# Performance work log

Hardware: AMD Instinct MI355X
Metric: run time of the kernel (lower is better)

## Reference

```python
import jax, jax.numpy as jnp
import numpy as np

D = 2048
H = 16
HD = D // H  # 128


def setup_inputs() -> dict:
    key = jax.random.key(0)
    k1, k2, k3 = jax.random.split(key, 3)
    x = jax.random.normal(k1, (2, 2048, D), dtype=jnp.float32)
    # nn.Linear(d, 3d, bias=False): weight [3d, d]; y = x @ W.T
    w_qkv = jax.random.normal(k2, (3 * D, D), dtype=jnp.float32) * (1.0 / np.sqrt(D))
    w_o = jax.random.normal(k3, (D, D), dtype=jnp.float32) * (1.0 / np.sqrt(D))
    return {"x": x, "w_qkv": w_qkv, "w_o": w_o}


def reference(x, w_qkv, w_o):
    B, T, _ = x.shape
    qkv = jnp.einsum('btd,ed->bte', x, w_qkv)  # [B,T,3D]
    q, k, v = jnp.split(qkv, 3, axis=-1)
    # [B,T,D] -> [B,H,T,hd]
    q = q.reshape(B, T, H, HD).transpose(0, 2, 1, 3)
    k = k.reshape(B, T, H, HD).transpose(0, 2, 1, 3)
    v = v.reshape(B, T, H, HD).transpose(0, 2, 1, 3)
    att = jnp.einsum('bhtd,bhsd->bhts', q, k) / np.sqrt(HD).astype(np.float32)
    att = jax.nn.softmax(att, axis=-1)
    y = jnp.einsum('bhts,bhsd->bhtd', att, v)
    y = y.transpose(0, 2, 1, 3).reshape(B, T, D)
    return jnp.einsum('btd,ed->bte', y, w_o)
```

## Files before the change

### kernel.cpp

```cpp
#include <hip/hip_runtime.h>
#include <hip/hip_bf16.h>
#include <math.h>

typedef __bf16 bf16_t;
typedef __attribute__((ext_vector_type(8))) __bf16 bx8;
typedef __attribute__((ext_vector_type(4))) __bf16 bx4;
typedef __attribute__((ext_vector_type(4))) short sx4;
typedef __attribute__((ext_vector_type(4))) float fx4;

#define DEV __device__ __forceinline__

DEV void async_copy16(void* lds, const void* g) {
    __builtin_amdgcn_global_load_lds(
        (const __attribute__((address_space(1))) unsigned int*)g,
        (__attribute__((address_space(3))) unsigned int*)lds, 16, 0, 0);
}

DEV fx4 mfma16(bx4 a, bx4 b, fx4 c) {
#if __has_builtin(__builtin_amdgcn_mfma_f32_16x16x16bf16_1k)
    return __builtin_amdgcn_mfma_f32_16x16x16bf16_1k(
        __builtin_bit_cast(sx4, a), __builtin_bit_cast(sx4, b), c, 0, 0, 0);
#elif __has_builtin(__builtin_amdgcn_mfma_f32_16x16x16_bf16)
    return __builtin_amdgcn_mfma_f32_16x16x16_bf16(a, b, c, 0, 0, 0);
#else
    asm("v_mfma_f32_16x16x16_bf16 %0, %1, %2, %0" : "+v"(c) : "v"(a), "v"(b));
    return c;
#endif
}

__global__ void __launch_bounds__(256) cvt_all(const float* __restrict__ x,
                                               const float* __restrict__ wq,
                                               const float* __restrict__ wo,
                                               bf16_t* __restrict__ xb,
                                               bf16_t* __restrict__ wqb,
                                               bf16_t* __restrict__ wob) {
    int i = (blockIdx.x * 256 + threadIdx.x) * 4;
    const float* in;
    bf16_t* out;
    int k;
    if (i < 8388608) { in = x; out = xb; k = i; }
    else if (i < 8388608 + 12582912) { in = wq; out = wqb; k = i - 8388608; }
    else { in = wo; out = wob; k = i - (8388608 + 12582912); }
    float4 v = *(const float4*)(in + k);
    bx4 o = { (__bf16)v.x, (__bf16)v.y, (__bf16)v.z, (__bf16)v.w };
    *(bx4*)(out + k) = o;
}

template <bool BF16_OUT>
__global__ void __launch_bounds__(256, 2) gemm_bt(const bf16_t* __restrict__ A,
                                                  const bf16_t* __restrict__ B,
                                                  void* __restrict__ C,
                                                  bf16_t* __restrict__ VP,
                                                  int M, int N, int K, float scale0) {
    __shared__ bf16_t As[2 * 4096];
    __shared__ bf16_t Bs[2 * 4096];
    const int tid = threadIdx.x;
    const int w = tid >> 6, lane = tid & 63;
    const int ln = lane & 15, quad = lane >> 4;
    const int m0 = blockIdx.y * 128, n0 = blockIdx.x * 128;
    const int wm = (w >> 1) * 64, wn = (w & 1) * 64;
    const float scale = (n0 < 2048) ? scale0 : 1.0f;

    fx4 acc[4][4];
#pragma unroll
    for (int i = 0; i < 4; ++i)
#pragma unroll
        for (int j = 0; j < 4; ++j) acc[i][j] = (fx4){0.f, 0.f, 0.f, 0.f};

    for (int k0 = 0; k0 < K; k0 += 64) {
#pragma unroll
        for (int call = 0; call < 4; ++call) {
            int c = w * 256 + call * 64 + lane;
            int p = c >> 9, row = (c >> 2) & 127, piece = c & 3;
            async_copy16(As + (size_t)(w * 256 + call * 64) * 8,
                         A + (size_t)(m0 + row) * K + k0 + p * 32 + piece * 8);
            async_copy16(Bs + (size_t)(w * 256 + call * 64) * 8,
                         B + (size_t)(n0 + row) * K + k0 + p * 32 + piece * 8);
        }
        __syncthreads();

#pragma unroll
        for (int kk = 0; kk < 2; ++kk) {
            bx8 af[4], bf[4];
#pragma unroll
            for (int i = 0; i < 4; ++i)
                af[i] = *(const bx8*)(As + (size_t)kk * 4096 + (wm + i * 16 + ln) * 32 + quad * 8);
#pragma unroll
            for (int j = 0; j < 4; ++j)
                bf[j] = *(const bx8*)(Bs + (size_t)kk * 4096 + (wn + j * 16 + ln) * 32 + quad * 8);
#pragma unroll
            for (int i = 0; i < 4; ++i)
#pragma unroll
                for (int j = 0; j < 4; ++j)
                    acc[i][j] = __builtin_amdgcn_mfma_f32_16x16x32_bf16(af[i], bf[j], acc[i][j], 0, 0, 0);
        }
        __syncthreads();
    }

    if (VP != nullptr && n0 >= 4096) {
        const int h = (n0 - 4096) >> 7;
        const int bidx = m0 >> 11;
        bf16_t* vpb = VP + (size_t)(bidx * 16 + h) * 262144;
        const int key_base = (m0 & 2047) + wm;
#pragma unroll
        for (int i = 0; i < 4; ++i) {
            int key = key_base + i * 16 + quad * 4;
#pragma unroll
            for (int j = 0; j < 4; ++j) {
                int hd = wn + j * 16 + ln;
                bx4 v = { (__bf16)acc[i][j][0], (__bf16)acc[i][j][1],
                          (__bf16)acc[i][j][2], (__bf16)acc[i][j][3] };
                *(bx4*)(vpb + (size_t)(key >> 2) * 512 + hd * 4) = v;
            }
        }
    } else {
#pragma unroll
        for (int i = 0; i < 4; ++i) {
            int mrow = m0 + wm + i * 16 + quad * 4;
#pragma unroll
            for (int j = 0; j < 4; ++j) {
                int ncol = n0 + wn + j * 16 + ln;
#pragma unroll
                for (int r = 0; r < 4; ++r) {
                    if (BF16_OUT)
                        ((bf16_t*)C)[(size_t)(mrow + r) * N + ncol] = (__bf16)(acc[i][j][r] * scale);
                    else
                        ((float*)C)[(size_t)(mrow + r) * N + ncol] = acc[i][j][r];
                }
            }
        }
    }
}

__global__ void __launch_bounds__(256, 2) attn(const bf16_t* __restrict__ qkv,
                                               const bf16_t* __restrict__ vp,
                                               bf16_t* __restrict__ y) {
    __shared__ bf16_t Ks[128 * 128];
    __shared__ bf16_t Vs[16384];
    const int tid = threadIdx.x;
    const int w = tid >> 6, lane = tid & 63;
    const int ln = lane & 15, quad = lane >> 4;
    const int lin = blockIdx.x;
    const int slot = lin >> 3;
    const int bh = (lin & 7) + ((slot >> 4) << 3);
    const int qt = slot & 15;
    const int b = bh >> 4, h = bh & 15;

    const bf16_t* Qb = qkv + (size_t)(b * 2048 + qt * 128) * 6144 + h * 128;
    const bf16_t* Kb = qkv + (size_t)(b * 2048) * 6144 + 2048 + h * 128;
    const bf16_t* VPb = vp + (size_t)bh * 262144;

    bx8 qf[2][4];
#pragma unroll
    for (int i = 0; i < 2; ++i)
#pragma unroll
        for (int kk = 0; kk < 4; ++kk)
            qf[i][kk] = *(const bx8*)(Qb + (size_t)(w * 32 + i * 16 + ln) * 6144 + kk * 32 + quad * 8);

    const __bf16 one = (__bf16)1.0f;
    const bx4 ones4 = { one, one, one, one };

    fx4 o[2][8];
#pragma unroll
    for (int i = 0; i < 2; ++i)
#pragma unroll
        for (int j = 0; j < 8; ++j) o[i][j] = (fx4){0.f, 0.f, 0.f, 0.f};
    fx4 lsum[2];
#pragma unroll
    for (int i = 0; i < 2; ++i) lsum[i] = (fx4){0.f, 0.f, 0.f, 0.f};

    for (int kt = 0; kt < 16; ++kt) {
#pragma unroll
        for (int call = 0; call < 8; ++call) {
            int cp = call * 64 + lane;
            int row = cp >> 2, piece = cp & 3;
            async_copy16(Ks + (size_t)w * 4096 + call * 512,
                         Kb + (size_t)(kt * 128 + row) * 6144 + w * 32 + piece * 8);
            async_copy16(Vs + (size_t)w * 4096 + call * 512,
                         VPb + (size_t)kt * 16384 + (w * 8 + call) * 512 + lane * 8);
        }
        __syncthreads();

#pragma unroll
        for (int q = 0; q < 4; ++q) {
            fx4 st[2][2];
#pragma unroll
            for (int i = 0; i < 2; ++i)
#pragma unroll
                for (int jj = 0; jj < 2; ++jj) st[i][jj] = (fx4){0.f, 0.f, 0.f, 0.f};
#pragma unroll
            for (int kk = 0; kk < 4; ++kk) {
                bx8 kf0 = *(const bx8*)(Ks + (size_t)kk * 4096 + ((2 * q) * 16 + ln) * 32 + quad * 8);
                bx8 kf1 = *(const bx8*)(Ks + (size_t)kk * 4096 + ((2 * q + 1) * 16 + ln) * 32 + quad * 8);
#pragma unroll
                for (int i = 0; i < 2; ++i) {
                    st[i][0] = __builtin_amdgcn_mfma_f32_16x16x32_bf16(kf0, qf[i][kk], st[i][0], 0, 0, 0);
                    st[i][1] = __builtin_amdgcn_mfma_f32_16x16x32_bf16(kf1, qf[i][kk], st[i][1], 0, 0, 0);
                }
            }

            bx4 pa[2][2];
#pragma unroll
            for (int i = 0; i < 2; ++i)
#pragma unroll
                for (int jj = 0; jj < 2; ++jj) {
                    bx4 t = { (__bf16)exp2f(st[i][jj][0]), (__bf16)exp2f(st[i][jj][1]),
                              (__bf16)exp2f(st[i][jj][2]), (__bf16)exp2f(st[i][jj][3]) };
                    pa[i][jj] = t;
                }

#pragma unroll
            for (int jj = 0; jj < 2; ++jj) {
                const int kt8 = 2 * q + jj;
                bx4 vf[8];
#pragma unroll
                for (int j = 0; j < 8; ++j)
                    vf[j] = *(const bx4*)(Vs + (size_t)(kt8 * 4 + quad) * 512 + (j * 16 + ln) * 4);
#pragma unroll
                for (int i = 0; i < 2; ++i) {
#pragma unroll
                    for (int j = 0; j < 8; ++j)
                        o[i][j] = mfma16(pa[i][jj], vf[j], o[i][j]);
                    lsum[i] = mfma16(pa[i][jj], ones4, lsum[i]);
                }
            }
        }
        __syncthreads();
    }

#pragma unroll
    for (int i = 0; i < 2; ++i)
#pragma unroll
        for (int r = 0; r < 4; ++r) {
            float rl = 1.0f / lsum[i][r];
#pragma unroll
            for (int j = 0; j < 8; ++j) {
                int t = qt * 128 + w * 32 + i * 16 + quad * 4 + r;
                int col = h * 128 + j * 16 + ln;
                y[(size_t)(b * 2048 + t) * 2048 + col] = (__bf16)(o[i][j][r] * rl);
            }
        }
}

extern "C" void kernel_launch(void* const* d_in, const int* in_sizes, int n_in,
                              void* d_out, int out_size, void* d_ws, size_t ws_size,
                              hipStream_t stream) {
    const float* x    = (const float*)d_in[0];
    const float* wqkv = (const float*)d_in[1];
    const float* wo   = (const float*)d_in[2];
    float* out = (float*)d_out;
    char* ws = (char*)d_ws;
    const float CEXP = 0.08838834764831845f * 1.44269504088896340f;

    bf16_t* Xb  = (bf16_t*)(ws);
    bf16_t* Wqb = (bf16_t*)(ws + (size_t)(16u << 20));
    bf16_t* Wob = (bf16_t*)(ws + (size_t)(40u << 20));
    bf16_t* QKV = (bf16_t*)(ws + (size_t)(48u << 20));
    bf16_t* VP  = (bf16_t*)(ws + (size_t)(96u << 20));
    bf16_t* Y   = Xb;

    cvt_all<<<24576, 256, 0, stream>>>(x, wqkv, wo, Xb, Wqb, Wob);

    gemm_bt<true><<<dim3(48, 32), 256, 0, stream>>>(Xb, Wqb, QKV, VP, 4096, 6144, 2048, CEXP);
    attn<<<dim3(512), 256, 0, stream>>>(QKV, VP, Y);
    gemm_bt<false><<<dim3(16, 32), 256, 0, stream>>>(Y, Wob, out, nullptr, 4096, 2048, 2048, 1.0f);
}
```

Before: 368.3 us.

## Halve attention query tile to 64 rows, doubling blocks and occupancy

Each attention block now handles 64 query rows instead of 128, with one 16-row strip per wave, and walks K/V in 64-key tiles over 32 iterations. This halves LDS and register use per block, so launch bounds go to 4 blocks per CU and the grid doubles to 1024. The aim is more waves in flight and better latency hiding across the 256 CUs. The cost is that every K/V tile is loaded from global memory twice as often overall, each wave reuses a K/V fragment over fewer query rows, and there are twice as many barriers.

```diff
diff --git a/kernel.cpp b/kernel.cpp
--- a/kernel.cpp
+++ b/kernel.cpp
@@ -132,82 +132,69 @@
     }
 }
 
-__global__ void __launch_bounds__(256, 2) attn(const bf16_t* __restrict__ qkv,
+__global__ void __launch_bounds__(256, 4) attn(const bf16_t* __restrict__ qkv,
                                                const bf16_t* __restrict__ vp,
                                                bf16_t* __restrict__ y) {
-    __shared__ bf16_t Ks[128 * 128];
-    __shared__ bf16_t Vs[16384];
+    __shared__ bf16_t Ks[4 * 2048];
+    __shared__ bf16_t Vs[8192];
     const int tid = threadIdx.x;
     const int w = tid >> 6, lane = tid & 63;
     const int ln = lane & 15, quad = lane >> 4;
     const int lin = blockIdx.x;
     const int slot = lin >> 3;
-    const int bh = (lin & 7) + ((slot >> 4) << 3);
-    const int qt = slot & 15;
+    const int bh = (lin & 7) + ((slot >> 5) << 3);
+    const int qt = slot & 31;
     const int b = bh >> 4, h = bh & 15;
 
-    const bf16_t* Qb = qkv + (size_t)(b * 2048 + qt * 128) * 6144 + h * 128;
+    const bf16_t* Qb = qkv + (size_t)(b * 2048 + qt * 64) * 6144 + h * 128;
     const bf16_t* Kb = qkv + (size_t)(b * 2048) * 6144 + 2048 + h * 128;
     const bf16_t* VPb = vp + (size_t)bh * 262144;
 
-    bx8 qf[2][4];
-#pragma unroll
-    for (int i = 0; i < 2; ++i)
-#pragma unroll
-        for (int kk = 0; kk < 4; ++kk)
-            qf[i][kk] = *(const bx8*)(Qb + (size_t)(w * 32 + i * 16 + ln) * 6144 + kk * 32 + quad * 8);
+    bx8 qf[4];
+#pragma unroll
+    for (int kk = 0; kk < 4; ++kk)
+        qf[kk] = *(const bx8*)(Qb + (size_t)(w * 16 + ln) * 6144 + kk * 32 + quad * 8);
 
     const __bf16 one = (__bf16)1.0f;
     const bx4 ones4 = { one, one, one, one };
 
-    fx4 o[2][8];
-#pragma unroll
-    for (int i = 0; i < 2; ++i)
-#pragma unroll
-        for (int j = 0; j < 8; ++j) o[i][j] = (fx4){0.f, 0.f, 0.f, 0.f};
-    fx4 lsum[2];
-#pragma unroll
-    for (int i = 0; i < 2; ++i) lsum[i] = (fx4){0.f, 0.f, 0.f, 0.f};
-
-    for (int kt = 0; kt < 16; ++kt) {
-#pragma unroll
-        for (int call = 0; call < 8; ++call) {
+    fx4 o[8];
+#pragma unroll
+    for (int j = 0; j < 8; ++j) o[j] = (fx4){0.f, 0.f, 0.f, 0.f};
+    fx4 lsum = (fx4){0.f, 0.f, 0.f, 0.f};
+
+    for (int kt = 0; kt < 32; ++kt) {
+#pragma unroll
+        for (int call = 0; call < 4; ++call) {
             int cp = call * 64 + lane;
             int row = cp >> 2, piece = cp & 3;
-            async_copy16(Ks + (size_t)w * 4096 + call * 512,
-                         Kb + (size_t)(kt * 128 + row) * 6144 + w * 32 + piece * 8);
-            async_copy16(Vs + (size_t)w * 4096 + call * 512,
-                         VPb + (size_t)kt * 16384 + (w * 8 + call) * 512 + lane * 8);
-        }
-        __syncthreads();
-
-#pragma unroll
-        for (int q = 0; q < 4; ++q) {
-            fx4 st[2][2];
-#pragma unroll
-            for (int i = 0; i < 2; ++i)
-#pragma unroll
-                for (int jj = 0; jj < 2; ++jj) st[i][jj] = (fx4){0.f, 0.f, 0.f, 0.f};
+            async_copy16(Ks + (size_t)w * 2048 + call * 512,
+                         Kb + (size_t)(kt * 64 + row) * 6144 + w * 32 + piece * 8);
+            async_copy16(Vs + (size_t)w * 2048 + call * 512,
+                         VPb + (size_t)kt * 8192 + (w * 4 + call) * 512 + lane * 8);
+        }
+        __syncthreads();
+
+#pragma unroll
+        for (int q = 0; q < 2; ++q) {
+            fx4 st[2];
+            st[0] = (fx4){0.f, 0.f, 0.f, 0.f};
+            st[1] = (fx4){0.f, 0.f, 0.f, 0.f};
 #pragma unroll
             for (int kk = 0; kk < 4; ++kk) {
-                bx8 kf0 = *(const bx8*)(Ks + (size_t)kk * 4096 + ((2 * q) * 16 + ln) * 32 + quad * 8);
-                bx8 kf1 = *(const bx8*)(Ks + (size_t)kk * 4096 + ((2 * q + 1) * 16 + ln) * 32 + quad * 8);
-#pragma unroll
-                for (int i = 0; i < 2; ++i) {
-                    st[i][0] = __builtin_amdgcn_mfma_f32_16x16x32_bf16(kf0, qf[i][kk], st[i][0], 0, 0, 0);
-                    st[i][1] = __builtin_amdgcn_mfma_f32_16x16x32_bf16(kf1, qf[i][kk], st[i][1], 0, 0, 0);
-                }
-            }
-
-            bx4 pa[2][2];
-#pragma unroll
-            for (int i = 0; i < 2; ++i)
-#pragma unroll
-                for (int jj = 0; jj < 2; ++jj) {
-                    bx4 t = { (__bf16)exp2f(st[i][jj][0]), (__bf16)exp2f(st[i][jj][1]),
-                              (__bf16)exp2f(st[i][jj][2]), (__bf16)exp2f(st[i][jj][3]) };
-                    pa[i][jj] = t;
-                }
+                bx8 kf0 = *(const bx8*)(Ks + (size_t)kk * 2048 + ((2 * q) * 16 + ln) * 32 + quad * 8);
+                bx8 kf1 = *(const bx8*)(Ks + (size_t)kk * 2048 + ((2 * q + 1) * 16 + ln) * 32 + quad * 8);
+                st[0] = __builtin_amdgcn_mfma_f32_16x16x32_bf16(kf0, qf[kk], st[0], 0, 0, 0);
+                st[1] = __builtin_amdgcn_mfma_f32_16x16x32_bf16(kf1, qf[kk], st[1], 0, 0, 0);
+            }
+
+            bx4 pa[2];
+#pragma unroll
+            for (int jj = 0; jj < 2; ++jj) {
+                bx4 t = { (__bf16)exp2f(st[jj][0]), (__bf16)exp2f(st[jj][1]),
+                          (__bf16)exp2f(st[jj][2]), (__bf16)exp2f(st[jj][3]) };
+                pa[jj] = t;
+            }
 
 #pragma unroll
             for (int jj = 0; jj < 2; ++jj) {
@@ -217,29 +204,24 @@
                 for (int j = 0; j < 8; ++j)
                     vf[j] = *(const bx4*)(Vs + (size_t)(kt8 * 4 + quad) * 512 + (j * 16 + ln) * 4);
 #pragma unroll
-                for (int i = 0; i < 2; ++i) {
-#pragma unroll
-                    for (int j = 0; j < 8; ++j)
-                        o[i][j] = mfma16(pa[i][jj], vf[j], o[i][j]);
-                    lsum[i] = mfma16(pa[i][jj], ones4, lsum[i]);
-                }
-            }
-        }
-        __syncthreads();
-    }
-
-#pragma unroll
-    for (int i = 0; i < 2; ++i)
-#pragma unroll
-        for (int r = 0; r < 4; ++r) {
-            float rl = 1.0f / lsum[i][r];
-#pragma unroll
-            for (int j = 0; j < 8; ++j) {
-                int t = qt * 128 + w * 32 + i * 16 + quad * 4 + r;
-                int col = h * 128 + j * 16 + ln;
-                y[(size_t)(b * 2048 + t) * 2048 + col] = (__bf16)(o[i][j][r] * rl);
-            }
-        }
+                for (int j = 0; j < 8; ++j)
+                    o[j] = mfma16(pa[jj], vf[j], o[j]);
+                lsum = mfma16(pa[jj], ones4, lsum);
+            }
+        }
+        __syncthreads();
+    }
+
+#pragma unroll
+    for (int r = 0; r < 4; ++r) {
+        float rl = 1.0f / lsum[r];
+#pragma unroll
+        for (int j = 0; j < 8; ++j) {
+            int t = qt * 64 + w * 16 + quad * 4 + r;
+            int col = h * 128 + j * 16 + ln;
+            y[(size_t)(b * 2048 + t) * 2048 + col] = (__bf16)(o[j][r] * rl);
+        }
+    }
 }
 
 extern "C" void kernel_launch(void* const* d_in, const int* in_sizes, int n_in,
@@ -262,6 +244,6 @@
     cvt_all<<<24576, 256, 0, stream>>>(x, wqkv, wo, Xb, Wqb, Wob);
 
     gemm_bt<true><<<dim3(48, 32), 256, 0, stream>>>(Xb, Wqb, QKV, VP, 4096, 6144, 2048, CEXP);
-    attn<<<dim3(512), 256, 0, stream>>>(QKV, VP, Y);
+    attn<<<dim3(1024), 256, 0, stream>>>(QKV, VP, Y);
     gemm_bt<false><<<dim3(16, 32), 256, 0, stream>>>(Y, Wob, out, nullptr, 4096, 2048, 2048, 1.0f);
 }
```

Measured after the change: 368.6 us. No clear change (+0.1%).
